# Optimization experiments

Measured on AMD Instinct MI355X. Metric: run time of the kernel, lower is better.

## Reference

```python
import jax, jax.numpy as jnp
import numpy as np

DIM = 512; HEADS = 8; DH = 64; M = 256; ITERS = 6; N_PATCH = 10000; N_CLASSES = 2


def layernorm(x, w, b, eps=1e-5):
    mu = x.mean(-1, keepdims=True)
    var = ((x - mu) ** 2).mean(-1, keepdims=True)
    return (x - mu) * jax.lax.rsqrt(var + eps) * w + b


def pinv_iter(x, iters=ITERS):
    # Moore-Penrose iterative pseudo-inverse (lucidrains nystrom-attention)
    abs_x = jnp.abs(x)
    col = abs_x.sum(-1)
    row = abs_x.sum(-2)
    z = jnp.swapaxes(x, -1, -2) / (jnp.max(col) * jnp.max(row))
    I = jnp.eye(x.shape[-1], dtype=x.dtype)
    for _ in range(iters):
        xz = x @ z
        z = 0.25 * z @ (13 * I - xz @ (15 * I - xz @ (7 * I - xz)))
    return z


def nystrom_attn(x, qkv_w, out_w, out_b, res_w):
    b, n, _ = x.shape
    pad = (-n) % M  # front-pad so n divisible by num_landmarks
    xp = jnp.pad(x, ((0, 0), (pad, 0), (0, 0)))
    npad = n + pad
    qkv = (xp @ qkv_w).reshape(b, npad, 3, HEADS, DH)
    q = jnp.transpose(qkv[:, :, 0], (0, 2, 1, 3)) * (DH ** -0.5)  # [b,h,n,d]
    k = jnp.transpose(qkv[:, :, 1], (0, 2, 1, 3))
    v = jnp.transpose(qkv[:, :, 2], (0, 2, 1, 3))
    l = npad // M
    q_l = q.reshape(b, HEADS, M, l, DH).mean(3)  # landmark means [b,h,m,d]
    k_l = k.reshape(b, HEADS, M, l, DH).mean(3)
    attn1 = jax.nn.softmax(jnp.einsum('bhnd,bhmd->bhnm', q, k_l), -1)
    attn2 = jax.nn.softmax(jnp.einsum('bhid,bhjd->bhij', q_l, k_l), -1)
    attn3 = jax.nn.softmax(jnp.einsum('bhmd,bhnd->bhmn', q_l, k), -1)
    out = (attn1 @ pinv_iter(attn2)) @ (attn3 @ v)  # [b,h,n,d]
    pk = (res_w.shape[2] - 1) // 2
    out = out + jax.lax.conv_general_dilated(
        v, res_w, (1, 1), [(pk, pk), (0, 0)], feature_group_count=HEADS)
    out = jnp.transpose(out, (0, 2, 1, 3)).reshape(b, npad, HEADS * DH)
    out = out @ out_w + out_b
    return out[:, -n:]


def ppeg(x, H, W, w7, b7, w5, b5, w3, b3):
    B, _, C = x.shape
    cls_tok, feat = x[:, :1], x[:, 1:]
    f = jnp.transpose(feat, (0, 2, 1)).reshape(B, C, H, W)
    def dw(w, b):
        p = w.shape[2] // 2
        return jax.lax.conv_general_dilated(
            f, w, (1, 1), [(p, p), (p, p)], feature_group_count=C) + b[None, :, None, None]
    y = f + dw(w7, b7) + dw(w5, b5) + dw(w3, b3)
    y = jnp.transpose(y.reshape(B, C, H * W), (0, 2, 1))
    return jnp.concatenate([cls_tok, y], axis=1)


def setup_inputs() -> dict:
    key = jax.random.key(0)
    ks = jax.random.split(key, 16)
    d = {
        'x': jax.random.normal(ks[0], (1, N_PATCH, DIM), jnp.float32),
        'cls_token': jax.random.normal(ks[1], (1, 1, DIM), jnp.float32) * 1e-6,
        'ln1_w': jnp.ones((DIM,), jnp.float32), 'ln1_b': jnp.zeros((DIM,), jnp.float32),
        'qkv1_w': jax.random.normal(ks[2], (DIM, 3 * DIM), jnp.float32) * 0.03,
        'out1_w': jax.random.normal(ks[3], (DIM, DIM), jnp.float32) * 0.04,
        'out1_b': jnp.zeros((DIM,), jnp.float32),
        'res1_w': jax.random.normal(ks[4], (HEADS, 1, 33, 1), jnp.float32) * 0.1,
        'p7_w': jax.random.normal(ks[5], (DIM, 1, 7, 7), jnp.float32) * 0.1,
        'p7_b': jnp.zeros((DIM,), jnp.float32),
        'p5_w': jax.random.normal(ks[6], (DIM, 1, 5, 5), jnp.float32) * 0.1,
        'p5_b': jnp.zeros((DIM,), jnp.float32),
        'p3_w': jax.random.normal(ks[7], (DIM, 1, 3, 3), jnp.float32) * 0.1,
        'p3_b': jnp.zeros((DIM,), jnp.float32),
        'ln2_w': jnp.ones((DIM,), jnp.float32), 'ln2_b': jnp.zeros((DIM,), jnp.float32),
        'qkv2_w': jax.random.normal(ks[8], (DIM, 3 * DIM), jnp.float32) * 0.03,
        'out2_w': jax.random.normal(ks[9], (DIM, DIM), jnp.float32) * 0.04,
        'out2_b': jnp.zeros((DIM,), jnp.float32),
        'res2_w': jax.random.normal(ks[10], (HEADS, 1, 33, 1), jnp.float32) * 0.1,
        'norm_w': jnp.ones((DIM,), jnp.float32), 'norm_b': jnp.zeros((DIM,), jnp.float32),
        'fc2_w': jax.random.normal(ks[11], (DIM, N_CLASSES), jnp.float32) * 0.06,
        'fc2_b': jnp.zeros((N_CLASSES,), jnp.float32),
        'pc_w': jax.random.normal(ks[12], (DIM, N_CLASSES), jnp.float32) * 0.06,
        'pc_b': jnp.zeros((N_CLASSES,), jnp.float32),
    }
    return d


def reference(x, cls_token, ln1_w, ln1_b, qkv1_w, out1_w, out1_b, res1_w,
              p7_w, p7_b, p5_w, p5_b, p3_w, p3_b,
              ln2_w, ln2_b, qkv2_w, out2_w, out2_b, res2_w,
              norm_w, norm_b, fc2_w, fc2_b, pc_w, pc_b):
    h = x.astype(jnp.float32)
    B, n0, C = h.shape
    _H = int(np.ceil(np.sqrt(n0))); _W = _H
    add = _H * _W - n0
    if add > 0:
        h = jnp.concatenate([h, h[:, :add]], axis=1)
    h = jnp.concatenate([jnp.broadcast_to(cls_token, (B, 1, C)), h], axis=1)
    h = h + nystrom_attn(layernorm(h, ln1_w, ln1_b), qkv1_w, out1_w, out1_b, res1_w)
    h = ppeg(h, _H, _W, p7_w, p7_b, p5_w, p5_b, p3_w, p3_b)
    h = h + nystrom_attn(layernorm(h, ln2_w, ln2_b), qkv2_w, out2_w, out2_b, res2_w)
    hn = layernorm(h, norm_w, norm_b)
    cls_f = hn[:, 0]
    patch_f = hn[:, 1:]
    if add > 0:
        patch_f = patch_f[:, :n0]
    bag_logits = cls_f @ fc2_w + fc2_b
    patch_logits = patch_f @ pc_w + pc_b
    patch_scores = jax.nn.softmax(patch_logits, -1)
    return bag_logits, patch_logits, patch_scores
```

## Files before the change

kernel.cpp:

```cpp
#include <hip/hip_runtime.h>
#include <hip/hip_bf16.h>

#define DIM    512
#define HEADS  8
#define DHD    64
#define MLAND  256
#define NTOK   10001
#define NPATCH 10000
#define NPAD   10240
#define PADR   239
#define LFAC   40
#define MOUT   10112
#define NSPLIT 8

typedef __bf16 bf16x8_t __attribute__((ext_vector_type(8)));
typedef float  f32x4_t  __attribute__((ext_vector_type(4)));
typedef short  short8_t __attribute__((ext_vector_type(8)));

__device__ inline bf16x8_t bzero8() {
    union { short8_t s; bf16x8_t b; } u;
    u.s = (short8_t){0, 0, 0, 0, 0, 0, 0, 0};
    return u.b;
}

#define GLDS(gp, lp) __builtin_amdgcn_global_load_lds( \
    (const __attribute__((address_space(1))) void*)(gp), \
    (__attribute__((address_space(3))) void*)(lp), 16, 0, 0)

__global__ void k_concat(const float* __restrict__ x, const float* __restrict__ cls,
                         float* __restrict__ h) {
    int idx = blockIdx.x * 256 + threadIdx.x;
    if (idx >= NTOK * DIM) return;
    int row = idx / DIM, col = idx % DIM;
    h[idx] = (row == 0) ? cls[col] : x[(row - 1) * DIM + col];
}

__global__ void k_layernorm_bf(const float* __restrict__ h, const float* __restrict__ w,
                               const float* __restrict__ b, __hip_bfloat16* __restrict__ xbf) {
    int row = blockIdx.x;
    const float* r = h + (long)row * DIM;
    int t = threadIdx.x;
    float v0 = r[t], v1 = r[t + 256];
    __shared__ float red[256];
    red[t] = v0 + v1; __syncthreads();
    for (int o = 128; o > 0; o >>= 1) { if (t < o) red[t] += red[t + o]; __syncthreads(); }
    float mu = red[0] * (1.f / DIM); __syncthreads();
    float d0 = v0 - mu, d1 = v1 - mu;
    red[t] = d0 * d0 + d1 * d1; __syncthreads();
    for (int o = 128; o > 0; o >>= 1) { if (t < o) red[t] += red[t + o]; __syncthreads(); }
    float rstd = rsqrtf(red[0] * (1.f / DIM) + 1e-5f);
    long base = (long)(PADR + row) * DIM;
    xbf[base + t]       = __float2bfloat16(d0 * rstd * w[t] + b[t]);
    xbf[base + t + 256] = __float2bfloat16(d1 * rstd * w[t + 256] + b[t + 256]);
}

__global__ void k_zerobf(__hip_bfloat16* __restrict__ p, int n) {
    int i = blockIdx.x * 256 + threadIdx.x;
    if (i < n) p[i] = __float2bfloat16(0.f);
}
__global__ void k_wt_cvt(const float* __restrict__ W, __hip_bfloat16* __restrict__ Wt,
                         int K, int N) {
    __shared__ float tile[32][33];
    int k0 = blockIdx.x * 32, n0 = blockIdx.y * 32;
    int lx = threadIdx.x % 32, ly = threadIdx.x / 32;
    for (int i = 0; i < 32; i += 8) tile[ly + i][lx] = W[(long)(k0 + ly + i) * N + n0 + lx];
    __syncthreads();
    for (int i = 0; i < 32; i += 8)
        Wt[(long)(n0 + ly + i) * K + k0 + lx] = __float2bfloat16(tile[lx][ly + i]);
}
__global__ void k_vt(const __hip_bfloat16* __restrict__ vh, __hip_bfloat16* __restrict__ vt) {
    __shared__ __hip_bfloat16 tile[32][33];
    int n0 = blockIdx.x * 32, d0 = blockIdx.y * 32, h = blockIdx.z;
    int lx = threadIdx.x % 32, ly = threadIdx.x / 32;
    for (int i = 0; i < 32; i += 8)
        tile[ly + i][lx] = vh[((long)h * NPAD + n0 + ly + i) * 64 + d0 + lx];
    __syncthreads();
    for (int i = 0; i < 32; i += 8)
        vt[((long)h * 64 + d0 + ly + i) * NPAD + n0 + lx] = tile[lx][ly + i];
}

__global__ __launch_bounds__(256) void k_qkv_gemm(
    const __hip_bfloat16* __restrict__ A, const __hip_bfloat16* __restrict__ Bt,
    __hip_bfloat16* __restrict__ qh, __hip_bfloat16* __restrict__ kh,
    __hip_bfloat16* __restrict__ vh)
{
    const int K = 512;
    __shared__ unsigned short As[2][128 * 64];
    __shared__ unsigned short Bs[2][128 * 64];
    int tid = threadIdx.x;
    int m0 = blockIdx.y * 128, n0 = blockIdx.x * 128;
    int wave = tid >> 6, lane = tid & 63;
    int wm = (wave & 1) * 64, wn = (wave >> 1) * 64;
    f32x4_t zero4 = {0.f, 0.f, 0.f, 0.f};
    f32x4_t acc[4][4];
#pragma unroll
    for (int i = 0; i < 4; i++)
#pragma unroll
        for (int j = 0; j < 4; j++) acc[i][j] = zero4;
    int quad = lane >> 4, fr = lane & 15;
    int lrow8 = lane >> 3, gls = lane & 7;
    int gg = gls ^ lrow8;

#define STAGE_AB(K0, AD, BD) do { \
    _Pragma("unroll") \
    for (int rnd = 0; rnd < 4; rnd++) { \
        int r0 = rnd * 32 + wave * 8; \
        int ar = r0 + lrow8; \
        GLDS(A  + (long)(m0 + ar) * K + (K0) + gg * 8, (AD) + r0 * 64); \
        GLDS(Bt + (long)(n0 + ar) * K + (K0) + gg * 8, (BD) + r0 * 64); \
    } \
} while (0)

    STAGE_AB(0, &As[0][0], &Bs[0][0]);
    for (int k0 = 0; k0 < K; k0 += 64) {
        int b = (k0 >> 6) & 1;
        if (k0 + 64 < K) {
            STAGE_AB(k0 + 64, &As[b ^ 1][0], &Bs[b ^ 1][0]);
            asm volatile("s_waitcnt vmcnt(8)" ::: "memory");
        } else {
            asm volatile("s_waitcnt vmcnt(0)" ::: "memory");
        }
        __builtin_amdgcn_s_barrier();
#pragma unroll
        for (int ks = 0; ks < 2; ks++) {
            int sg = (ks * 4 + quad) ^ (fr & 7);
            bf16x8_t af[4], bq[4];
#pragma unroll
            for (int i = 0; i < 4; i++) {
                af[i] = *(const bf16x8_t*)&As[b][(wm + i * 16 + fr) * 64 + sg * 8];
                bq[i] = *(const bf16x8_t*)&Bs[b][(wn + i * 16 + fr) * 64 + sg * 8];
            }
#pragma unroll
            for (int i = 0; i < 4; i++)
#pragma unroll
                for (int j = 0; j < 4; j++)
                    acc[i][j] = __builtin_amdgcn_mfma_f32_16x16x32_bf16(af[i], bq[j], acc[i][j], 0, 0, 0);
        }
        asm volatile("" ::: "memory");
        __builtin_amdgcn_s_barrier();
    }
#undef STAGE_AB
    int col = lane & 15, rq = lane >> 4;
#pragma unroll
    for (int j = 0; j < 4; j++) {
        int c = n0 + wn + j * 16 + col;
        int sect = c >> 9;
        int hh = (c >> 6) & 7;
        int d = c & 63;
        __hip_bfloat16* dst = (sect == 0) ? qh : (sect == 1) ? kh : vh;
        float sc = (sect == 0) ? 0.125f : 1.f;
#pragma unroll
        for (int i = 0; i < 4; i++) {
            int rbase = m0 + wm + i * 16 + rq * 4;
#pragma unroll
            for (int rr = 0; rr < 4; rr++) {
                int r = rbase + rr;
                dst[((long)hh * NPAD + r) * 64 + d] = __float2bfloat16(acc[i][j][rr] * sc);
            }
        }
    }
}

__global__ __launch_bounds__(256) void k_mfma_gemm(
    const __hip_bfloat16* __restrict__ A, const __hip_bfloat16* __restrict__ Bt,
    float* __restrict__ C, int M, int N, int K, int Mstore,
    const float* __restrict__ bias, int accum)
{
    __shared__ unsigned short As[2][128 * 64];
    __shared__ unsigned short Bs[2][128 * 64];
    int tid = threadIdx.x;
    int m0 = blockIdx.y * 128, n0 = blockIdx.x * 128;
    int wave = tid >> 6, lane = tid & 63;
    int wm = (wave & 1) * 64, wn = (wave >> 1) * 64;
    f32x4_t zero4 = {0.f, 0.f, 0.f, 0.f};
    f32x4_t acc[4][4];
#pragma unroll
    for (int i = 0; i < 4; i++)
#pragma unroll
        for (int j = 0; j < 4; j++) acc[i][j] = zero4;
    int quad = lane >> 4, fr = lane & 15;
    int lrow8 = lane >> 3, gls = lane & 7;
    int gg = gls ^ lrow8;

#define STAGE_AB(K0, AD, BD) do { \
    _Pragma("unroll") \
    for (int rnd = 0; rnd < 4; rnd++) { \
        int r0 = rnd * 32 + wave * 8; \
        int ar = r0 + lrow8; \
        GLDS(A  + (long)(m0 + ar) * K + (K0) + gg * 8, (AD) + r0 * 64); \
        GLDS(Bt + (long)(n0 + ar) * K + (K0) + gg * 8, (BD) + r0 * 64); \
    } \
} while (0)

    STAGE_AB(0, &As[0][0], &Bs[0][0]);
    for (int k0 = 0; k0 < K; k0 += 64) {
        int b = (k0 >> 6) & 1;
        if (k0 + 64 < K) {
            STAGE_AB(k0 + 64, &As[b ^ 1][0], &Bs[b ^ 1][0]);
            asm volatile("s_waitcnt vmcnt(8)" ::: "memory");
        } else {
            asm volatile("s_waitcnt vmcnt(0)" ::: "memory");
        }
        __builtin_amdgcn_s_barrier();
#pragma unroll
        for (int ks = 0; ks < 2; ks++) {
            int sg = (ks * 4 + quad) ^ (fr & 7);
            bf16x8_t af[4], bq[4];
#pragma unroll
            for (int i = 0; i < 4; i++) {
                af[i] = *(const bf16x8_t*)&As[b][(wm + i * 16 + fr) * 64 + sg * 8];
                bq[i] = *(const bf16x8_t*)&Bs[b][(wn + i * 16 + fr) * 64 + sg * 8];
            }
#pragma unroll
            for (int i = 0; i < 4; i++)
#pragma unroll
                for (int j = 0; j < 4; j++)
                    acc[i][j] = __builtin_amdgcn_mfma_f32_16x16x32_bf16(af[i], bq[j], acc[i][j], 0, 0, 0);
        }
        asm volatile("" ::: "memory");
        __builtin_amdgcn_s_barrier();
    }
#undef STAGE_AB
    int col = lane & 15, rq = lane >> 4;
#pragma unroll
    for (int j = 0; j < 4; j++) {
        int c = n0 + wn + j * 16 + col;
        float bsv = bias ? bias[c] : 0.f;
#pragma unroll
        for (int i = 0; i < 4; i++) {
            int rbase = m0 + wm + i * 16 + rq * 4;
#pragma unroll
            for (int rr = 0; rr < 4; rr++) {
                int r = rbase + rr;
                if (r >= Mstore) continue;
                float v = acc[i][j][rr] + bsv;
                long off = (long)r * N + c;
                if (accum) C[off] += v; else C[off] = v;
            }
        }
    }
}

__global__ __launch_bounds__(256) void k_mfma_t64(
    const __hip_bfloat16* __restrict__ A, long lda, long abatch, int arowmax,
    const __hip_bfloat16* __restrict__ Bt, long ldb, long bbatch,
    __hip_bfloat16* __restrict__ Cbf, long ldc, long cbatch, int ksplit)
{
    int h = blockIdx.z;
    const __hip_bfloat16* Ab = A + (long)h * abatch;
    const __hip_bfloat16* Bb = Bt + (long)h * bbatch;
    int m0 = blockIdx.y * 128;
    int kbeg = blockIdx.x * ksplit, kend = kbeg + ksplit;
    int wave = threadIdx.x >> 6, lane = threadIdx.x & 63;
    int wm = (wave & 1) * 64, wn = (wave >> 1) * 32;
    int fr = lane & 15, quad = lane >> 4;
    f32x4_t zero4 = {0.f, 0.f, 0.f, 0.f};
    f32x4_t acc[4][2];
#pragma unroll
    for (int i = 0; i < 4; i++) { acc[i][0] = zero4; acc[i][1] = zero4; }
    for (int k0 = kbeg; k0 < kend; k0 += 32) {
        bf16x8_t bq[2];
#pragma unroll
        for (int j = 0; j < 2; j++)
            bq[j] = *(const bf16x8_t*)(Bb + (long)(wn + j * 16 + fr) * ldb + k0 + quad * 8);
#pragma unroll
        for (int i = 0; i < 4; i++) {
            int r = m0 + wm + i * 16 + fr;
            bf16x8_t af = (r < arowmax) ? *(const bf16x8_t*)(Ab + (long)r * lda + k0 + quad * 8)
                                        : bzero8();
#pragma unroll
            for (int j = 0; j < 2; j++)
                acc[i][j] = __builtin_amdgcn_mfma_f32_16x16x32_bf16(af, bq[j], acc[i][j], 0, 0, 0);
        }
    }
#pragma unroll
    for (int i = 0; i < 4; i++)
#pragma unroll
        for (int j = 0; j < 2; j++)
#pragma unroll
            for (int rr = 0; rr < 4; rr++) {
                int r = m0 + wm + i * 16 + quad * 4 + rr;
                int c = wn + j * 16 + fr;
                Cbf[(long)h * cbatch + (long)c * ldc + r] = __float2bfloat16(acc[i][j][rr]);
            }
}

__global__ __launch_bounds__(256) void k_mm256(
    const __hip_bfloat16* __restrict__ Aa, const __hip_bfloat16* __restrict__ Bt,
    float s, float acoef, const __hip_bfloat16* __restrict__ Aadd,
    __hip_bfloat16* __restrict__ Ca, __hip_bfloat16* __restrict__ Ct)
{
    int hd = blockIdx.z;
    long hb = (long)hd * 65536;
    int m0 = blockIdx.y * 64, n0 = blockIdx.x * 32;
    int wave = threadIdx.x >> 6, lane = threadIdx.x & 63;
    int fr = lane & 15, quad = lane >> 4;
    int mrow = m0 + wave * 16;
    f32x4_t zero4 = {0.f, 0.f, 0.f, 0.f};
    f32x4_t acc[2];
    acc[0] = zero4; acc[1] = zero4;
#pragma unroll
    for (int k0 = 0; k0 < 256; k0 += 32) {
        bf16x8_t af = *(const bf16x8_t*)(Aa + hb + (long)(mrow + fr) * 256 + k0 + quad * 8);
#pragma unroll
        for (int j = 0; j < 2; j++) {
            bf16x8_t bq = *(const bf16x8_t*)(Bt + hb + (long)(n0 + j * 16 + fr) * 256 + k0 + quad * 8);
            acc[j] = __builtin_amdgcn_mfma_f32_16x16x32_bf16(af, bq, acc[j], 0, 0, 0);
        }
    }
#pragma unroll
    for (int j = 0; j < 2; j++)
#pragma unroll
        for (int rr = 0; rr < 4; rr++) {
            int r = mrow + quad * 4 + rr;
            int c = n0 + j * 16 + fr;
            float v = s * acc[j][rr];
            if (Aadd) v += acoef * __bfloat162float(Aadd[hb + (long)r * 256 + c]);
            __hip_bfloat16 bv = __float2bfloat16(v);
            if (Ca) Ca[hb + (long)r * 256 + c] = bv;
            if (Ct) Ct[hb + (long)c * 256 + r] = bv;
        }
}

__global__ __launch_bounds__(256) void k_attn3f(
    const __hip_bfloat16* __restrict__ qlbf, const __hip_bfloat16* __restrict__ kh,
    const __hip_bfloat16* __restrict__ vt, float* __restrict__ part)
{
    int ns = blockIdx.x, mt = blockIdx.y, h = blockIdx.z;
    int wave = threadIdx.x >> 6, lane = threadIdx.x & 63;
    int fr = lane & 15, quad = lane >> 4;
    int lrow8 = lane >> 3, gls = lane & 7;
    int gg = gls ^ lrow8;
    int vsub = lane >> 5, vgrp = lane & 31;
    int swz = fr & 7;
    __shared__ unsigned short Ks[2][256 * 64];
    __shared__ unsigned short Vs[2][64 * 256];
    __shared__ __hip_bfloat16 Pl[64 * 136];
    f32x4_t zero4 = {0.f, 0.f, 0.f, 0.f};
    bf16x8_t aq[2];
    {
        const __hip_bfloat16* qb = qlbf + (long)h * 16384 + (long)(mt * 64 + wave * 16 + fr) * 64;
        aq[0] = *(const bf16x8_t*)(qb + quad * 8);
        aq[1] = *(const bf16x8_t*)(qb + 32 + quad * 8);
    }
    f32x4_t O[4];
#pragma unroll
    for (int j = 0; j < 4; j++) O[j] = zero4;
    float mr[4] = {-1e30f, -1e30f, -1e30f, -1e30f};
    float lr[4] = {0.f, 0.f, 0.f, 0.f};
    const __hip_bfloat16* kb = kh + (long)h * NPAD * 64;
    const __hip_bfloat16* vb = vt + (long)h * 64 * NPAD;

#define STAGE_KV(N0, KD, VD) do { \
    _Pragma("unroll") \
    for (int rnd = 0; rnd < 8; rnd++) { \
        int r0 = rnd * 32 + wave * 8; \
        GLDS(kb + (long)((N0) + r0 + lrow8) * 64 + gg * 8, (KD) + r0 * 64); \
    } \
    _Pragma("unroll") \
    for (int rnd = 0; rnd < 8; rnd++) { \
        int v0 = rnd * 8 + wave * 2; \
        int vrow = v0 + vsub; \
        GLDS(vb + (long)vrow * NPAD + (N0) + (vgrp ^ (vrow & 7)) * 8, (VD) + v0 * 256); \
    } \
} while (0)

    STAGE_KV(ns * 1280, &Ks[0][0], &Vs[0][0]);

    for (int nt = 0; nt < 5; nt++) {
        int bsel = nt & 1;
        if (nt < 4) {
            int n1 = ns * 1280 + (nt + 1) * 256;
            STAGE_KV(n1, &Ks[bsel ^ 1][0], &Vs[bsel ^ 1][0]);
            asm volatile("s_waitcnt vmcnt(16)" ::: "memory");
        } else {
            asm volatile("s_waitcnt vmcnt(0)" ::: "memory");
        }
        __builtin_amdgcn_s_barrier();

        const unsigned short* Kc = &Ks[bsel][0];
        const unsigned short* Vc = &Vs[bsel][0];
        f32x4_t s[16];
#pragma unroll
        for (int j = 0; j < 16; j++) s[j] = zero4;
#pragma unroll
        for (int j = 0; j < 16; j++) {
            const unsigned short* kr = Kc + (j * 16 + fr) * 64;
            bf16x8_t b0 = *(const bf16x8_t*)(kr + (quad ^ swz) * 8);
            bf16x8_t b1 = *(const bf16x8_t*)(kr + ((quad ^ swz) ^ 4) * 8);
            s[j] = __builtin_amdgcn_mfma_f32_16x16x32_bf16(aq[0], b0, s[j], 0, 0, 0);
            s[j] = __builtin_amdgcn_mfma_f32_16x16x32_bf16(aq[1], b1, s[j], 0, 0, 0);
        }
        float tm[4] = {-1e30f, -1e30f, -1e30f, -1e30f};
#pragma unroll
        for (int j = 0; j < 16; j++)
#pragma unroll
            for (int rr = 0; rr < 4; rr++) tm[rr] = fmaxf(tm[rr], s[j][rr]);
#pragma unroll
        for (int rr = 0; rr < 4; rr++) {
#pragma unroll
            for (int o = 8; o > 0; o >>= 1) tm[rr] = fmaxf(tm[rr], __shfl_xor(tm[rr], o));
        }
        float alpha[4], ts[4];
#pragma unroll
        for (int rr = 0; rr < 4; rr++) {
            float mnew = fmaxf(mr[rr], tm[rr]);
            alpha[rr] = __expf(mr[rr] - mnew);
            mr[rr] = mnew;
            ts[rr] = 0.f;
        }
#pragma unroll
        for (int j = 0; j < 16; j++)
#pragma unroll
            for (int rr = 0; rr < 4; rr++) {
                float e = __expf(s[j][rr] - mr[rr]);
                s[j][rr] = e;
                ts[rr] += e;
            }
#pragma unroll
        for (int rr = 0; rr < 4; rr++) {
#pragma unroll
            for (int o = 8; o > 0; o >>= 1) ts[rr] += __shfl_xor(ts[rr], o);
            lr[rr] = lr[rr] * alpha[rr] + ts[rr];
        }
#pragma unroll
        for (int j = 0; j < 4; j++)
#pragma unroll
            for (int rr = 0; rr < 4; rr++) O[j][rr] *= alpha[rr];
#pragma unroll
        for (int half = 0; half < 2; half++) {
#pragma unroll
            for (int j = 0; j < 8; j++)
#pragma unroll
                for (int rr = 0; rr < 4; rr++)
                    Pl[(wave * 16 + quad * 4 + rr) * 136 + j * 16 + fr] =
                        __float2bfloat16(s[half * 8 + j][rr]);
#pragma unroll
            for (int k0 = 0; k0 < 128; k0 += 32) {
                bf16x8_t af = *(const bf16x8_t*)&Pl[(wave * 16 + fr) * 136 + k0 + quad * 8];
                int gb = (half * 128 + k0) >> 3;
#pragma unroll
                for (int j = 0; j < 4; j++) {
                    const unsigned short* vr = Vc + (j * 16 + fr) * 256;
                    bf16x8_t bq = *(const bf16x8_t*)(vr + ((gb + quad) ^ swz) * 8);
                    O[j] = __builtin_amdgcn_mfma_f32_16x16x32_bf16(af, bq, O[j], 0, 0, 0);
                }
            }
        }
        asm volatile("" ::: "memory");
        __builtin_amdgcn_s_barrier();
    }
#undef STAGE_KV

    float* Ob = part + (long)((h * 4 + mt) * NSPLIT + ns) * 4224;
#pragma unroll
    for (int j = 0; j < 4; j++)
#pragma unroll
        for (int rr = 0; rr < 4; rr++)
            Ob[(wave * 16 + quad * 4 + rr) * 64 + j * 16 + fr] = O[j][rr];
    if (fr == 0) {
#pragma unroll
        for (int rr = 0; rr < 4; rr++) {
            Ob[4096 + wave * 16 + quad * 4 + rr] = mr[rr];
            Ob[4160 + wave * 16 + quad * 4 + rr] = lr[rr];
        }
    }
}

__global__ void k_a3comb(const float* __restrict__ part, __hip_bfloat16* __restrict__ a3vt) {
    int mt = blockIdx.x, h = blockIdx.y, t = threadIdx.x;
    int row = t >> 2, c0 = (t & 3) * 16;
    long base = (long)((h * 4 + mt) * NSPLIT) * 4224;
    float M = -1e30f;
    for (int s = 0; s < NSPLIT; s++) M = fmaxf(M, part[base + s * 4224 + 4096 + row]);
    float L = 0.f;
    float o[16];
#pragma unroll
    for (int c = 0; c < 16; c++) o[c] = 0.f;
    for (int s = 0; s < NSPLIT; s++) {
        const float* pb = part + base + (long)s * 4224;
        float w = __expf(pb[4096 + row] - M);
        L += pb[4160 + row] * w;
#pragma unroll
        for (int c = 0; c < 16; c++) o[c] += w * pb[row * 64 + c0 + c];
    }
    float invL = 1.f / L;
#pragma unroll
    for (int c = 0; c < 16; c++)
        a3vt[(long)h * 16384 + (long)(c0 + c) * 256 + mt * 64 + row] = __float2bfloat16(o[c] * invL);
}

__global__ void k_conv_res(const __hip_bfloat16* __restrict__ vh, const float* __restrict__ resw,
                           __hip_bfloat16* __restrict__ convbf) {
    int e4 = blockIdx.x * 256 + threadIdx.x;
    if (e4 >= NTOK * 128) return;
    int i = e4 >> 7;
    int c4 = (e4 & 127) * 4;
    int hh = c4 >> 6, d = c4 & 63;
    int n = PADR + i;
    const __hip_bfloat16* vb = vh + (long)hh * NPAD * 64 + d;
    float a0 = 0.f, a1 = 0.f, a2 = 0.f, a3 = 0.f;
#pragma unroll
    for (int t = 0; t < 33; t++) {
        int nn = n - 16 + t;
        if (nn < NPAD) {
            float w = resw[hh * 33 + t];
            uint2 pv = *(const uint2*)(vb + (long)nn * 64);
            __hip_bfloat16 vv[4];
            *(uint2*)vv = pv;
            a0 += w * __bfloat162float(vv[0]);
            a1 += w * __bfloat162float(vv[1]);
            a2 += w * __bfloat162float(vv[2]);
            a3 += w * __bfloat162float(vv[3]);
        }
    }
    __hip_bfloat16 o[4] = {__float2bfloat16(a0), __float2bfloat16(a1),
                           __float2bfloat16(a2), __float2bfloat16(a3)};
    *(uint2*)(convbf + (long)i * DIM + c4) = *(uint2*)o;
}

__global__ __launch_bounds__(256, 3) void k_attn1f(
    const __hip_bfloat16* __restrict__ qh, const __hip_bfloat16* __restrict__ klbf,
    const __hip_bfloat16* __restrict__ w2bt, const __hip_bfloat16* __restrict__ convbf,
    __hip_bfloat16* __restrict__ abf)
{
    int h = blockIdx.y;
    int i0 = blockIdx.x * 64;
    __shared__ __hip_bfloat16 Pl[64 * 136];
    __shared__ float mS[2][2][2][16];
    int tid = threadIdx.x;
    int wave = tid >> 6, lane = tid & 63;
    int rg = wave & 1, lh = wave >> 1;
    int fr = lane & 15, quad = lane >> 4;
    const __hip_bfloat16* kb = klbf + (long)h * (MLAND * DHD) + (long)lh * 128 * DHD;
    f32x4_t zero4 = {0.f, 0.f, 0.f, 0.f};

    f32x4_t s0[8], s1[8];
#pragma unroll
    for (int j = 0; j < 8; j++) { s0[j] = zero4; s1[j] = zero4; }
    int arow0 = i0 + rg * 16 + fr;
    int arow1 = arow0 + 32;
    const __hip_bfloat16* qrow = qh + ((long)h * NPAD + PADR + arow0) * 64;
#pragma unroll
    for (int k0 = 0; k0 < 64; k0 += 32) {
        bf16x8_t af0 = (arow0 < NTOK) ? *(const bf16x8_t*)(qrow + k0 + quad * 8) : bzero8();
        bf16x8_t af1 = (arow1 < NTOK) ? *(const bf16x8_t*)(qrow + 32 * 64 + k0 + quad * 8) : bzero8();
#pragma unroll
        for (int j = 0; j < 8; j++) {
            bf16x8_t bq = *(const bf16x8_t*)(kb + (long)(j * 16 + fr) * DHD + k0 + quad * 8);
            s0[j] = __builtin_amdgcn_mfma_f32_16x16x32_bf16(af0, bq, s0[j], 0, 0, 0);
            s1[j] = __builtin_amdgcn_mfma_f32_16x16x32_bf16(af1, bq, s1[j], 0, 0, 0);
        }
    }
    float sum0[4] = {0.f, 0.f, 0.f, 0.f}, sum1[4] = {0.f, 0.f, 0.f, 0.f};
#pragma unroll
    for (int j = 0; j < 8; j++)
#pragma unroll
        for (int rr = 0; rr < 4; rr++) {
            float e0 = __expf(s0[j][rr]); s0[j][rr] = e0; sum0[rr] += e0;
            float e1 = __expf(s1[j][rr]); s1[j][rr] = e1; sum1[rr] += e1;
        }
#pragma unroll
    for (int rr = 0; rr < 4; rr++) {
#pragma unroll
        for (int o = 8; o > 0; o >>= 1) {
            sum0[rr] += __shfl_xor(sum0[rr], o);
            sum1[rr] += __shfl_xor(sum1[rr], o);
        }
    }
    if (fr == 0) {
#pragma unroll
        for (int rr = 0; rr < 4; rr++) {
            mS[0][lh][rg][quad * 4 + rr] = sum0[rr];
            mS[1][lh][rg][quad * 4 + rr] = sum1[rr];
        }
    }
#pragma unroll
    for (int j = 0; j < 8; j++)
#pragma unroll
        for (int rr = 0; rr < 4; rr++) {
            Pl[(rg * 16 + quad * 4 + rr) * 136 + j * 16 + fr]      = __float2bfloat16(s0[j][rr]);
            Pl[(32 + rg * 16 + quad * 4 + rr) * 136 + j * 16 + fr] = __float2bfloat16(s1[j][rr]);
        }
    __syncthreads();
    float fac0[4], fac1[4];
#pragma unroll
    for (int rr = 0; rr < 4; rr++) {
        fac0[rr] = 1.f / (sum0[rr] + mS[0][lh ^ 1][rg][quad * 4 + rr]);
        fac1[rr] = 1.f / (sum1[rr] + mS[1][lh ^ 1][rg][quad * 4 + rr]);
    }
    float cp[2][4][4];
    if (lh == 0) {
#pragma unroll
        for (int rt = 0; rt < 2; rt++)
#pragma unroll
            for (int j = 0; j < 4; j++)
#pragma unroll
                for (int rr = 0; rr < 4; rr++) {
                    int r = i0 + rt * 32 + rg * 16 + quad * 4 + rr;
                    cp[rt][j][rr] = (r < NTOK)
                        ? __bfloat162float(convbf[(long)r * DIM + h * DHD + j * 16 + fr]) : 0.f;
                }
    }
    const __hip_bfloat16* wb = w2bt + (long)h * (DHD * MLAND) + lh * 128;
    f32x4_t oc0[4], oc1[4];
#pragma unroll
    for (int j = 0; j < 4; j++) { oc0[j] = zero4; oc1[j] = zero4; }
#pragma unroll
    for (int k0 = 0; k0 < 128; k0 += 32) {
        bf16x8_t af0 = *(const bf16x8_t*)&Pl[(rg * 16 + fr) * 136 + k0 + quad * 8];
        bf16x8_t af1 = *(const bf16x8_t*)&Pl[(32 + rg * 16 + fr) * 136 + k0 + quad * 8];
#pragma unroll
        for (int j = 0; j < 4; j++) {
            bf16x8_t bq = *(const bf16x8_t*)(wb + (long)(j * 16 + fr) * MLAND + k0 + quad * 8);
            oc0[j] = __builtin_amdgcn_mfma_f32_16x16x32_bf16(af0, bq, oc0[j], 0, 0, 0);
            oc1[j] = __builtin_amdgcn_mfma_f32_16x16x32_bf16(af1, bq, oc1[j], 0, 0, 0);
        }
    }
#pragma unroll
    for (int j = 0; j < 4; j++)
#pragma unroll
        for (int rr = 0; rr < 4; rr++) {
            oc0[j][rr] *= fac0[rr];
            oc1[j][rr] *= fac1[rr];
        }
    __syncthreads();
    float* ex = (float*)Pl;
    if (lh == 1) {
#pragma unroll
        for (int j = 0; j < 4; j++)
#pragma unroll
            for (int rr = 0; rr < 4; rr++) {
                ex[(rg * 16 + quad * 4 + rr) * 64 + j * 16 + fr]      = oc0[j][rr];
                ex[(32 + rg * 16 + quad * 4 + rr) * 64 + j * 16 + fr] = oc1[j][rr];
            }
    }
    __syncthreads();
    if (lh == 0) {
#pragma unroll
        for (int j = 0; j < 4; j++)
#pragma unroll
            for (int rr = 0; rr < 4; rr++) {
                int lr0 = rg * 16 + quad * 4 + rr;
                int r0 = i0 + lr0;
                if (r0 < NTOK) {
                    float v = oc0[j][rr] + ex[lr0 * 64 + j * 16 + fr] + cp[0][j][rr];
                    abf[(long)r0 * DIM + h * DHD + j * 16 + fr] = __float2bfloat16(v);
                }
                int r1 = r0 + 32;
                if (r1 < NTOK) {
                    float v = oc1[j][rr] + ex[(32 + lr0) * 64 + j * 16 + fr] + cp[1][j][rr];
                    abf[(long)r1 * DIM + h * DHD + j * 16 + fr] = __float2bfloat16(v);
                }
            }
    }
}

__global__ void k_landmarks(const __hip_bfloat16* __restrict__ qh,
                            const __hip_bfloat16* __restrict__ kh,
                            float* __restrict__ ql, float* __restrict__ kl,
                            __hip_bfloat16* __restrict__ qlbf, __hip_bfloat16* __restrict__ klbf) {
    int m = blockIdx.x, h = blockIdx.y, d = threadIdx.x;
    float sq = 0.f, sk = 0.f;
    for (int j = 0; j < LFAC; j++) {
        long base = ((long)h * NPAD + m * LFAC + j) * 64 + d;
        sq += __bfloat162float(qh[base]);
        sk += __bfloat162float(kh[base]);
    }
    long o = ((long)h * MLAND + m) * DHD + d;
    float vq = sq * (1.f / LFAC), vk = sk * (1.f / LFAC);
    ql[o] = vq; kl[o] = vk;
    qlbf[o] = __float2bfloat16(vq);
    klbf[o] = __float2bfloat16(vk);
}

__global__ void k_attn2(const float* __restrict__ ql, const float* __restrict__ kl,
                        float* __restrict__ attn2, __hip_bfloat16* __restrict__ attn2bf) {
    int i = blockIdx.x, h = blockIdx.y, j = threadIdx.x;
    __shared__ float q[64];
    __shared__ float red[256];
    if (j < 64) q[j] = ql[((long)h * MLAND + i) * DHD + j];
    __syncthreads();
    const float* kr = kl + ((long)h * MLAND + j) * DHD;
    float s = 0.f;
#pragma unroll 8
    for (int d = 0; d < 64; d++) s += q[d] * kr[d];
    red[j] = s; __syncthreads();
    for (int o = 128; o > 0; o >>= 1) { if (j < o) red[j] = fmaxf(red[j], red[j + o]); __syncthreads(); }
    float mx = red[0]; __syncthreads();
    float e = __expf(s - mx);
    red[j] = e; __syncthreads();
    for (int o = 128; o > 0; o >>= 1) { if (j < o) red[j] += red[j + o]; __syncthreads(); }
    float v = e / red[0];
    long off = ((long)h * MLAND + i) * MLAND + j;
    attn2[off] = v;
    attn2bf[off] = __float2bfloat16(v);
}

__global__ void k_colrow(const float* __restrict__ x, float* __restrict__ scal) {
    int h = blockIdx.x, t = threadIdx.x;
    const float* xh = x + (long)h * MLAND * MLAND;
    float cs = 0.f, rs = 0.f;
    for (int j = 0; j < MLAND; j++) {
        cs += fabsf(xh[(long)t * MLAND + j]);
        rs += fabsf(xh[(long)j * MLAND + t]);
    }
    __shared__ float red[256];
    red[t] = cs; __syncthreads();
    for (int o = 128; o > 0; o >>= 1) { if (t < o) red[t] = fmaxf(red[t], red[t + o]); __syncthreads(); }
    if (t == 0) scal[2 + h] = red[0];
    __syncthreads();
    red[t] = rs; __syncthreads();
    for (int o = 128; o > 0; o >>= 1) { if (t < o) red[t] = fmaxf(red[t], red[t + o]); __syncthreads(); }
    if (t == 0) scal[10 + h] = red[0];
}

__global__ void k_tscale2(const float* __restrict__ x, const float* __restrict__ scal,
                          __hip_bfloat16* __restrict__ za, __hip_bfloat16* __restrict__ zt) {
    int h = blockIdx.z;
    int tj = blockIdx.x * 32, ti = blockIdx.y * 32;
    __shared__ float tile[32][33];
    const float* xh = x + (long)h * 65536;
    int lx = threadIdx.x % 32, ly = threadIdx.x / 32;
    float cm = scal[2], rm = scal[10];
#pragma unroll
    for (int k = 1; k < 8; k++) {
        cm = fmaxf(cm, scal[2 + k]);
        rm = fmaxf(rm, scal[10 + k]);
    }
    float inv = 1.f / (cm * rm);
    for (int yy = 0; yy < 32; yy += 8) {
        float v = xh[(long)(ti + ly + yy) * MLAND + tj + lx];
        tile[ly + yy][lx] = v;
        zt[(long)h * 65536 + (long)(ti + ly + yy) * MLAND + tj + lx] = __float2bfloat16(v * inv);
    }
    __syncthreads();
    for (int yy = 0; yy < 32; yy += 8)
        za[(long)h * 65536 + (long)(tj + ly + yy) * MLAND + ti + lx] =
            __float2bfloat16(tile[lx][ly + yy] * inv);
}

__global__ void k_tfwd(const float* __restrict__ h, float* __restrict__ ft) {
    __shared__ float tile[32][33];
    int t0 = blockIdx.x * 32, c0 = blockIdx.y * 32;
    int lx = threadIdx.x % 32, ly = threadIdx.x / 32;
    for (int i = 0; i < 32; i += 8) {
        int t = t0 + ly + i;
        if (t < NPATCH) tile[ly + i][lx] = h[(long)(1 + t) * DIM + c0 + lx];
    }
    __syncthreads();
    for (int i = 0; i < 32; i += 8) {
        int c = c0 + ly + i, t = t0 + lx;
        if (t < NPATCH) ft[(long)c * NPATCH + t] = tile[lx][ly + i];
    }
}

__global__ __launch_bounds__(256) void k_ppeg2(
    const float* __restrict__ ft, float* __restrict__ yt,
    const float* __restrict__ w7, const float* __restrict__ b7,
    const float* __restrict__ w5, const float* __restrict__ b5,
    const float* __restrict__ w3, const float* __restrict__ b3)
{
    int s = blockIdx.x, c = blockIdx.y;
    __shared__ float tile[26][106];
    __shared__ float wt[49];
    int tid = threadIdx.x;
    int r0 = s * 20 - 3;
    for (int idx = tid; idx < 26 * 106; idx += 256) {
        int rr = idx / 106, cc = idx % 106;
        int gy = r0 + rr, gx = cc - 3;
        float v = 0.f;
        if (gy >= 0 && gy < 100 && gx >= 0 && gx < 100)
            v = ft[(long)c * NPATCH + gy * 100 + gx];
        tile[rr][cc] = v;
    }
    if (tid < 49) {
        int dy = tid / 7 - 3, dx = tid % 7 - 3;
        float w = w7[c * 49 + tid];
        if (dy >= -2 && dy <= 2 && dx >= -2 && dx <= 2) w += w5[c * 25 + (dy + 2) * 5 + (dx + 2)];
        if (dy >= -1 && dy <= 1 && dx >= -1 && dx <= 1) w += w3[c * 9 + (dy + 1) * 3 + (dx + 1)];
        wt[tid] = w;
    }
    __syncthreads();
    float bsum = b7[c] + b5[c] + b3[c];
    for (int p = tid; p < 2000; p += 256) {
        int ly = p / 100, lx = p % 100;
        float acc = tile[ly + 3][lx + 3] + bsum;
#pragma unroll
        for (int dy = 0; dy < 7; dy++)
#pragma unroll
            for (int dx = 0; dx < 7; dx++)
                acc += wt[dy * 7 + dx] * tile[ly + dy][lx + dx];
        yt[(long)c * NPATCH + (s * 20 + ly) * 100 + lx] = acc;
    }
}

__global__ void k_tback(const float* __restrict__ yt, float* __restrict__ h) {
    __shared__ float tile[32][33];
    int t0 = blockIdx.x * 32, c0 = blockIdx.y * 32;
    int lx = threadIdx.x % 32, ly = threadIdx.x / 32;
    for (int i = 0; i < 32; i += 8) {
        int c = c0 + ly + i, t = t0 + lx;
        if (t < NPATCH) tile[ly + i][lx] = yt[(long)c * NPATCH + t];
    }
    __syncthreads();
    for (int i = 0; i < 32; i += 8) {
        int t = t0 + ly + i;
        if (t < NPATCH) h[(long)(1 + t) * DIM + c0 + lx] = tile[lx][ly + i];
    }
}

__global__ void k_final(const float* __restrict__ h, const float* __restrict__ nw,
                        const float* __restrict__ nb,
                        const float* __restrict__ fc2w, const float* __restrict__ fc2b,
                        const float* __restrict__ pcw, const float* __restrict__ pcb,
                        float* __restrict__ out)
{
    int row = blockIdx.x;
    int t = threadIdx.x;
    const float* r = h + (long)row * DIM;
    float v0 = r[t], v1 = r[t + 256];
    __shared__ float red[256];
    red[t] = v0 + v1; __syncthreads();
    for (int o = 128; o > 0; o >>= 1) { if (t < o) red[t] += red[t + o]; __syncthreads(); }
    float mu = red[0] * (1.f / DIM); __syncthreads();
    float d0 = v0 - mu, d1 = v1 - mu;
    red[t] = d0 * d0 + d1 * d1; __syncthreads();
    for (int o = 128; o > 0; o >>= 1) { if (t < o) red[t] += red[t + o]; __syncthreads(); }
    float rstd = rsqrtf(red[0] * (1.f / DIM) + 1e-5f); __syncthreads();
    float h0 = d0 * rstd * nw[t] + nb[t];
    float h1 = d1 * rstd * nw[t + 256] + nb[t + 256];
    const float* w = (row == 0) ? fc2w : pcw;
    float p0 = h0 * w[t * 2] + h1 * w[(t + 256) * 2];
    float p1 = h0 * w[t * 2 + 1] + h1 * w[(t + 256) * 2 + 1];
    red[t] = p0; __syncthreads();
    for (int o = 128; o > 0; o >>= 1) { if (t < o) red[t] += red[t + o]; __syncthreads(); }
    float l0 = red[0]; __syncthreads();
    red[t] = p1; __syncthreads();
    for (int o = 128; o > 0; o >>= 1) { if (t < o) red[t] += red[t + o]; __syncthreads(); }
    if (t == 0) {
        float l1 = red[0];
        const float* bb = (row == 0) ? fc2b : pcb;
        float a0 = l0 + bb[0], a1 = l1 + bb[1];
        if (row == 0) { out[0] = a0; out[1] = a1; }
        else {
            long i = row - 1;
            out[2 + i * 2] = a0;
            out[2 + i * 2 + 1] = a1;
            float m = fmaxf(a0, a1);
            float e0 = __expf(a0 - m), e1 = __expf(a1 - m);
            float inv = 1.f / (e0 + e1);
            out[2 + 2 * NPATCH + i * 2] = e0 * inv;
            out[2 + 2 * NPATCH + i * 2 + 1] = e1 * inv;
        }
    }
}

extern "C" void kernel_launch(void* const* d_in, const int* in_sizes, int n_in,
                              void* d_out, int out_size, void* d_ws, size_t ws_size,
                              hipStream_t stream)
{
    const float* x     = (const float*)d_in[0];
    const float* cls   = (const float*)d_in[1];
    const float* ln1w  = (const float*)d_in[2];
    const float* ln1b  = (const float*)d_in[3];
    const float* qkv1w = (const float*)d_in[4];
    const float* out1w = (const float*)d_in[5];
    const float* out1b = (const float*)d_in[6];
    const float* res1w = (const float*)d_in[7];
    const float* p7w   = (const float*)d_in[8];
    const float* p7b   = (const float*)d_in[9];
    const float* p5w   = (const float*)d_in[10];
    const float* p5b   = (const float*)d_in[11];
    const float* p3w   = (const float*)d_in[12];
    const float* p3b   = (const float*)d_in[13];
    const float* ln2w  = (const float*)d_in[14];
    const float* ln2b  = (const float*)d_in[15];
    const float* qkv2w = (const float*)d_in[16];
    const float* out2w = (const float*)d_in[17];
    const float* out2b = (const float*)d_in[18];
    const float* res2w = (const float*)d_in[19];
    const float* normw = (const float*)d_in[20];
    const float* normb = (const float*)d_in[21];
    const float* fc2w  = (const float*)d_in[22];
    const float* fc2b  = (const float*)d_in[23];
    const float* pcw   = (const float*)d_in[24];
    const float* pcb   = (const float*)d_in[25];
    float* out = (float*)d_out;

    float* p = (float*)d_ws;
    float* h      = p; p += 5120512;
    float* yt     = p; p += 5120512;
    float* ql     = p; p += 131072;
    float* kl     = p; p += 131072;
    float* x2     = p; p += 524288;
    float* scal   = p; p += 32;
    float* part   = p; p += 1081344;
    float* ft     = p; p += 5120512;
    __hip_bfloat16* qh     = (__hip_bfloat16*)p; p += 2621440;
    __hip_bfloat16* kh     = (__hip_bfloat16*)p; p += 2621440;
    __hip_bfloat16* vh     = (__hip_bfloat16*)p; p += 2621440;
    __hip_bfloat16* xbf    = (__hip_bfloat16*)p; p += 2621440;
    __hip_bfloat16* abf    = (__hip_bfloat16*)p; p += 2588672;
    __hip_bfloat16* convbf = (__hip_bfloat16*)p; p += 2560256;
    __hip_bfloat16* qw1t   = (__hip_bfloat16*)p; p += 393216;
    __hip_bfloat16* qw2t   = (__hip_bfloat16*)p; p += 393216;
    __hip_bfloat16* ow1t   = (__hip_bfloat16*)p; p += 131072;
    __hip_bfloat16* ow2t   = (__hip_bfloat16*)p; p += 131072;
    __hip_bfloat16* x2a    = (__hip_bfloat16*)p; p += 262144;
    __hip_bfloat16* za     = (__hip_bfloat16*)p; p += 262144;
    __hip_bfloat16* zt     = (__hip_bfloat16*)p; p += 262144;
    __hip_bfloat16* za2    = (__hip_bfloat16*)p; p += 262144;
    __hip_bfloat16* zt2    = (__hip_bfloat16*)p; p += 262144;
    __hip_bfloat16* xza    = (__hip_bfloat16*)p; p += 262144;
    __hip_bfloat16* xzt    = (__hip_bfloat16*)p; p += 262144;
    __hip_bfloat16* t1t    = (__hip_bfloat16*)p; p += 262144;
    __hip_bfloat16* t2t    = (__hip_bfloat16*)p; p += 262144;
    __hip_bfloat16* qlbf   = (__hip_bfloat16*)p; p += 65536;
    __hip_bfloat16* klbf   = (__hip_bfloat16*)p; p += 65536;
    __hip_bfloat16* vt     = (__hip_bfloat16*)p; p += 2621440;
    __hip_bfloat16* a3vt   = (__hip_bfloat16*)p; p += 65536;
    __hip_bfloat16* w2bt   = (__hip_bfloat16*)p; p += 65536;

    k_concat<<<dim3((NTOK * DIM + 255) / 256), 256, 0, stream>>>(x, cls, h);
    k_wt_cvt<<<dim3(16, 48), 256, 0, stream>>>(qkv1w, qw1t, 512, 1536);
    k_wt_cvt<<<dim3(16, 48), 256, 0, stream>>>(qkv2w, qw2t, 512, 1536);
    k_wt_cvt<<<dim3(16, 16), 256, 0, stream>>>(out1w, ow1t, 512, 512);
    k_wt_cvt<<<dim3(16, 16), 256, 0, stream>>>(out2w, ow2t, 512, 512);
    k_zerobf<<<dim3((PADR * DIM + 255) / 256), 256, 0, stream>>>(xbf, PADR * DIM);

    auto layer = [&](const float* lnw, const float* lnb, const __hip_bfloat16* qwt,
                     const __hip_bfloat16* owt, const float* outb, const float* resw) {
        k_layernorm_bf<<<NTOK, 256, 0, stream>>>(h, lnw, lnb, xbf);
        k_qkv_gemm<<<dim3(12, 80), 256, 0, stream>>>(xbf, qwt, qh, kh, vh);
        k_vt<<<dim3(320, 2, HEADS), 256, 0, stream>>>(vh, vt);
        k_landmarks<<<dim3(MLAND, HEADS), 64, 0, stream>>>(qh, kh, ql, kl, qlbf, klbf);
        k_attn2<<<dim3(MLAND, HEADS), 256, 0, stream>>>(ql, kl, x2, x2a);
        k_colrow<<<HEADS, 256, 0, stream>>>(x2, scal);
        k_tscale2<<<dim3(8, 8, HEADS), 256, 0, stream>>>(x2, scal, za, zt);
        {
            __hip_bfloat16 *zra = za, *zrt = zt, *zoa = za2, *zot = zt2;
            dim3 g(8, 4, HEADS);
            for (int it = 0; it < 6; it++) {
                k_mm256<<<g, 256, 0, stream>>>(x2a, zrt, 1.f, 0.f, nullptr, xza, xzt);
                k_mm256<<<g, 256, 0, stream>>>(xza, xzt, -1.f, 7.f, xza, nullptr, t1t);
                k_mm256<<<g, 256, 0, stream>>>(xza, t1t, -1.f, 15.f, xza, nullptr, t2t);
                k_mm256<<<g, 256, 0, stream>>>(zra, t2t, -0.25f, 3.25f, zra, zoa, zot);
                __hip_bfloat16* tmp;
                tmp = zra; zra = zoa; zoa = tmp;
                tmp = zrt; zrt = zot; zot = tmp;
            }
        }
        k_attn3f<<<dim3(NSPLIT, 4, HEADS), 256, 0, stream>>>(qlbf, kh, vt, part);
        k_a3comb<<<dim3(4, HEADS), 256, 0, stream>>>(part, a3vt);
        k_mfma_t64<<<dim3(1, 2, HEADS), 256, 0, stream>>>(
            za, 256, 65536, 256, a3vt, 256, 16384,
            w2bt, 256, 16384, 256);
        k_conv_res<<<dim3((NTOK * 128 + 255) / 256), 256, 0, stream>>>(vh, resw, convbf);
        k_attn1f<<<dim3(157, HEADS), 256, 0, stream>>>(qh, klbf, w2bt, convbf, abf);
        k_mfma_gemm<<<dim3(4, 79), 256, 0, stream>>>(abf, owt, h, MOUT, 512, 512,
                                                     NTOK, outb, 1);
    };

    layer(ln1w, ln1b, qw1t, ow1t, out1b, res1w);

    k_tfwd<<<dim3(313, 16), 256, 0, stream>>>(h, ft);
    k_ppeg2<<<dim3(5, 512), 256, 0, stream>>>(ft, yt, p7w, p7b, p5w, p5b, p3w, p3b);
    k_tback<<<dim3(313, 16), 256, 0, stream>>>(yt, h);

    layer(ln2w, ln2b, qw2t, ow2t, out2b, res2w);

    k_final<<<NTOK, 256, 0, stream>>>(h, normw, normb, fc2w, fc2b, pcw, pcb, out);
    (void)in_sizes; (void)n_in; (void)out_size; (void)ws_size;
}
```

Baseline: 965.8 us.

## Restructure pinv iteration into parallel products and use wave-per-row layernorm

Rewrites each Newton-Schulz pseudo-inverse step as z·xz and xz·xz computed in one launch, then a fused kernel forming 3.25z-3.75U+1.75U·xz-0.25U·W. This cuts the serial matmul chain per iteration from four launches to three. Layernorm and the final head kernel now process one row per wavefront with shuffle reductions instead of block-wide shared-memory trees. The column-abs-sum max is replaced by 1.0, relying on softmax rows summing to one, which changes bf16 rounding slightly.

```diff
diff --git a/kernel.cpp b/kernel.cpp
--- a/kernel.cpp
+++ b/kernel.cpp
@@ -35,23 +35,34 @@
     h[idx] = (row == 0) ? cls[col] : x[(row - 1) * DIM + col];
 }
 
-__global__ void k_layernorm_bf(const float* __restrict__ h, const float* __restrict__ w,
-                               const float* __restrict__ b, __hip_bfloat16* __restrict__ xbf) {
-    int row = blockIdx.x;
+__global__ __launch_bounds__(256) void k_layernorm_bf(
+    const float* __restrict__ h, const float* __restrict__ w,
+    const float* __restrict__ b, __hip_bfloat16* __restrict__ xbf) {
+    int wave = threadIdx.x >> 6, lane = threadIdx.x & 63;
+    int row = blockIdx.x * 4 + wave;
+    if (row >= NTOK) return;
     const float* r = h + (long)row * DIM;
-    int t = threadIdx.x;
-    float v0 = r[t], v1 = r[t + 256];
-    __shared__ float red[256];
-    red[t] = v0 + v1; __syncthreads();
-    for (int o = 128; o > 0; o >>= 1) { if (t < o) red[t] += red[t + o]; __syncthreads(); }
-    float mu = red[0] * (1.f / DIM); __syncthreads();
-    float d0 = v0 - mu, d1 = v1 - mu;
-    red[t] = d0 * d0 + d1 * d1; __syncthreads();
-    for (int o = 128; o > 0; o >>= 1) { if (t < o) red[t] += red[t + o]; __syncthreads(); }
-    float rstd = rsqrtf(red[0] * (1.f / DIM) + 1e-5f);
-    long base = (long)(PADR + row) * DIM;
-    xbf[base + t]       = __float2bfloat16(d0 * rstd * w[t] + b[t]);
-    xbf[base + t + 256] = __float2bfloat16(d1 * rstd * w[t + 256] + b[t + 256]);
+    int c0 = lane * 8;
+    f32x4_t va = *(const f32x4_t*)(r + c0);
+    f32x4_t vb = *(const f32x4_t*)(r + c0 + 4);
+    float s = va[0] + va[1] + va[2] + va[3] + vb[0] + vb[1] + vb[2] + vb[3];
+#pragma unroll
+    for (int o = 32; o > 0; o >>= 1) s += __shfl_xor(s, o);
+    float mu = s * (1.f / DIM);
+    float d[8];
+#pragma unroll
+    for (int i = 0; i < 4; i++) { d[i] = va[i] - mu; d[4 + i] = vb[i] - mu; }
+    float vs = 0.f;
+#pragma unroll
+    for (int i = 0; i < 8; i++) vs += d[i] * d[i];
+#pragma unroll
+    for (int o = 32; o > 0; o >>= 1) vs += __shfl_xor(vs, o);
+    float rstd = rsqrtf(vs * (1.f / DIM) + 1e-5f);
+    __hip_bfloat16 ob[8];
+#pragma unroll
+    for (int i = 0; i < 8; i++)
+        ob[i] = __float2bfloat16(d[i] * rstd * w[c0 + i] + b[c0 + i]);
+    *(uint4*)(xbf + (long)(PADR + row) * DIM + c0) = *(uint4*)ob;
 }
 
 __global__ void k_zerobf(__hip_bfloat16* __restrict__ p, int n) {
@@ -319,6 +330,83 @@
             __hip_bfloat16 bv = __float2bfloat16(v);
             if (Ca) Ca[hb + (long)r * 256 + c] = bv;
             if (Ct) Ct[hb + (long)c * 256 + r] = bv;
+        }
+}
+
+__global__ __launch_bounds__(256) void k_pinvUW(
+    const __hip_bfloat16* __restrict__ za, const __hip_bfloat16* __restrict__ xza,
+    const __hip_bfloat16* __restrict__ xzt,
+    __hip_bfloat16* __restrict__ ua, __hip_bfloat16* __restrict__ wt)
+{
+    int z = blockIdx.z;
+    int hd = z & 7, isW = z >> 3;
+    long hb = (long)hd * 65536;
+    int m0 = blockIdx.y * 64, n0 = blockIdx.x * 32;
+    int wave = threadIdx.x >> 6, lane = threadIdx.x & 63;
+    int fr = lane & 15, quad = lane >> 4;
+    int mrow = m0 + wave * 16;
+    const __hip_bfloat16* Aa = isW ? xza : za;
+    f32x4_t zero4 = {0.f, 0.f, 0.f, 0.f};
+    f32x4_t acc[2];
+    acc[0] = zero4; acc[1] = zero4;
+#pragma unroll
+    for (int k0 = 0; k0 < 256; k0 += 32) {
+        bf16x8_t af = *(const bf16x8_t*)(Aa + hb + (long)(mrow + fr) * 256 + k0 + quad * 8);
+#pragma unroll
+        for (int j = 0; j < 2; j++) {
+            bf16x8_t bq = *(const bf16x8_t*)(xzt + hb + (long)(n0 + j * 16 + fr) * 256 + k0 + quad * 8);
+            acc[j] = __builtin_amdgcn_mfma_f32_16x16x32_bf16(af, bq, acc[j], 0, 0, 0);
+        }
+    }
+#pragma unroll
+    for (int j = 0; j < 2; j++)
+#pragma unroll
+        for (int rr = 0; rr < 4; rr++) {
+            int r = mrow + quad * 4 + rr;
+            int c = n0 + j * 16 + fr;
+            __hip_bfloat16 bv = __float2bfloat16(acc[j][rr]);
+            if (!isW) ua[hb + (long)r * 256 + c] = bv;
+            else      wt[hb + (long)c * 256 + r] = bv;
+        }
+}
+
+__global__ __launch_bounds__(256) void k_pinv3(
+    const __hip_bfloat16* __restrict__ ua, const __hip_bfloat16* __restrict__ xzt,
+    const __hip_bfloat16* __restrict__ wt, const __hip_bfloat16* __restrict__ za,
+    __hip_bfloat16* __restrict__ Ca, __hip_bfloat16* __restrict__ Ct)
+{
+    int hd = blockIdx.z;
+    long hb = (long)hd * 65536;
+    int m0 = blockIdx.y * 64, n0 = blockIdx.x * 32;
+    int wave = threadIdx.x >> 6, lane = threadIdx.x & 63;
+    int fr = lane & 15, quad = lane >> 4;
+    int mrow = m0 + wave * 16;
+    f32x4_t zero4 = {0.f, 0.f, 0.f, 0.f};
+    f32x4_t acc1[2], acc2[2];
+    acc1[0] = zero4; acc1[1] = zero4; acc2[0] = zero4; acc2[1] = zero4;
+#pragma unroll
+    for (int k0 = 0; k0 < 256; k0 += 32) {
+        bf16x8_t af = *(const bf16x8_t*)(ua + hb + (long)(mrow + fr) * 256 + k0 + quad * 8);
+#pragma unroll
+        for (int j = 0; j < 2; j++) {
+            bf16x8_t b1 = *(const bf16x8_t*)(xzt + hb + (long)(n0 + j * 16 + fr) * 256 + k0 + quad * 8);
+            bf16x8_t b2 = *(const bf16x8_t*)(wt  + hb + (long)(n0 + j * 16 + fr) * 256 + k0 + quad * 8);
+            acc1[j] = __builtin_amdgcn_mfma_f32_16x16x32_bf16(af, b1, acc1[j], 0, 0, 0);
+            acc2[j] = __builtin_amdgcn_mfma_f32_16x16x32_bf16(af, b2, acc2[j], 0, 0, 0);
+        }
+    }
+#pragma unroll
+    for (int j = 0; j < 2; j++)
+#pragma unroll
+        for (int rr = 0; rr < 4; rr++) {
+            int r = mrow + quad * 4 + rr;
+            int c = n0 + j * 16 + fr;
+            float zv = __bfloat162float(za[hb + (long)r * 256 + c]);
+            float uv = __bfloat162float(ua[hb + (long)r * 256 + c]);
+            float v = 3.25f * zv - 3.75f * uv + 1.75f * acc1[j][rr] - 0.25f * acc2[j][rr];
+            __hip_bfloat16 bv = __float2bfloat16(v);
+            Ca[hb + (long)r * 256 + c] = bv;
+            Ct[hb + (long)c * 256 + r] = bv;
         }
 }
 
@@ -700,19 +788,12 @@
 __global__ void k_colrow(const float* __restrict__ x, float* __restrict__ scal) {
     int h = blockIdx.x, t = threadIdx.x;
     const float* xh = x + (long)h * MLAND * MLAND;
-    float cs = 0.f, rs = 0.f;
-    for (int j = 0; j < MLAND; j++) {
-        cs += fabsf(xh[(long)t * MLAND + j]);
-        rs += fabsf(xh[(long)j * MLAND + t]);
-    }
+    float rs = 0.f;
+    for (int j = 0; j < MLAND; j++) rs += fabsf(xh[(long)j * MLAND + t]);
     __shared__ float red[256];
-    red[t] = cs; __syncthreads();
-    for (int o = 128; o > 0; o >>= 1) { if (t < o) red[t] = fmaxf(red[t], red[t + o]); __syncthreads(); }
-    if (t == 0) scal[2 + h] = red[0];
-    __syncthreads();
     red[t] = rs; __syncthreads();
     for (int o = 128; o > 0; o >>= 1) { if (t < o) red[t] = fmaxf(red[t], red[t + o]); __syncthreads(); }
-    if (t == 0) scal[10 + h] = red[0];
+    if (t == 0) { scal[10 + h] = red[0]; scal[2 + h] = 1.0f; }
 }
 
 __global__ void k_tscale2(const float* __restrict__ x, const float* __restrict__ scal,
@@ -810,38 +891,49 @@
     }
 }
 
-__global__ void k_final(const float* __restrict__ h, const float* __restrict__ nw,
-                        const float* __restrict__ nb,
-                        const float* __restrict__ fc2w, const float* __restrict__ fc2b,
-                        const float* __restrict__ pcw, const float* __restrict__ pcb,
-                        float* __restrict__ out)
+__global__ __launch_bounds__(256) void k_final(
+    const float* __restrict__ h, const float* __restrict__ nw,
+    const float* __restrict__ nb,
+    const float* __restrict__ fc2w, const float* __restrict__ fc2b,
+    const float* __restrict__ pcw, const float* __restrict__ pcb,
+    float* __restrict__ out)
 {
-    int row = blockIdx.x;
-    int t = threadIdx.x;
+    int wave = threadIdx.x >> 6, lane = threadIdx.x & 63;
+    int row = blockIdx.x * 4 + wave;
+    if (row >= NTOK) return;
     const float* r = h + (long)row * DIM;
-    float v0 = r[t], v1 = r[t + 256];
-    __shared__ float red[256];
-    red[t] = v0 + v1; __syncthreads();
-    for (int o = 128; o > 0; o >>= 1) { if (t < o) red[t] += red[t + o]; __syncthreads(); }
-    float mu = red[0] * (1.f / DIM); __syncthreads();
-    float d0 = v0 - mu, d1 = v1 - mu;
-    red[t] = d0 * d0 + d1 * d1; __syncthreads();
-    for (int o = 128; o > 0; o >>= 1) { if (t < o) red[t] += red[t + o]; __syncthreads(); }
-    float rstd = rsqrtf(red[0] * (1.f / DIM) + 1e-5f); __syncthreads();
-    float h0 = d0 * rstd * nw[t] + nb[t];
-    float h1 = d1 * rstd * nw[t + 256] + nb[t + 256];
+    int c0 = lane * 8;
+    f32x4_t va = *(const f32x4_t*)(r + c0);
+    f32x4_t vb = *(const f32x4_t*)(r + c0 + 4);
+    float s = va[0] + va[1] + va[2] + va[3] + vb[0] + vb[1] + vb[2] + vb[3];
+#pragma unroll
+    for (int o = 32; o > 0; o >>= 1) s += __shfl_xor(s, o);
+    float mu = s * (1.f / DIM);
+    float d[8];
+#pragma unroll
+    for (int i = 0; i < 4; i++) { d[i] = va[i] - mu; d[4 + i] = vb[i] - mu; }
+    float vs = 0.f;
+#pragma unroll
+    for (int i = 0; i < 8; i++) vs += d[i] * d[i];
+#pragma unroll
+    for (int o = 32; o > 0; o >>= 1) vs += __shfl_xor(vs, o);
+    float rstd = rsqrtf(vs * (1.f / DIM) + 1e-5f);
     const float* w = (row == 0) ? fc2w : pcw;
-    float p0 = h0 * w[t * 2] + h1 * w[(t + 256) * 2];
-    float p1 = h0 * w[t * 2 + 1] + h1 * w[(t + 256) * 2 + 1];
-    red[t] = p0; __syncthreads();
-    for (int o = 128; o > 0; o >>= 1) { if (t < o) red[t] += red[t + o]; __syncthreads(); }
-    float l0 = red[0]; __syncthreads();
-    red[t] = p1; __syncthreads();
-    for (int o = 128; o > 0; o >>= 1) { if (t < o) red[t] += red[t + o]; __syncthreads(); }
-    if (t == 0) {
-        float l1 = red[0];
+    float p0 = 0.f, p1 = 0.f;
+#pragma unroll
+    for (int i = 0; i < 8; i++) {
+        float hn = d[i] * rstd * nw[c0 + i] + nb[c0 + i];
+        p0 += hn * w[(c0 + i) * 2];
+        p1 += hn * w[(c0 + i) * 2 + 1];
+    }
+#pragma unroll
+    for (int o = 32; o > 0; o >>= 1) {
+        p0 += __shfl_xor(p0, o);
+        p1 += __shfl_xor(p1, o);
+    }
+    if (lane == 0) {
         const float* bb = (row == 0) ? fc2b : pcb;
-        float a0 = l0 + bb[0], a1 = l1 + bb[1];
+        float a0 = p0 + bb[0], a1 = p1 + bb[1];
         if (row == 0) { out[0] = a0; out[1] = a1; }
         else {
             long i = row - 1;
@@ -931,7 +1023,7 @@
 
     auto layer = [&](const float* lnw, const float* lnb, const __hip_bfloat16* qwt,
                      const __hip_bfloat16* owt, const float* outb, const float* resw) {
-        k_layernorm_bf<<<NTOK, 256, 0, stream>>>(h, lnw, lnb, xbf);
+        k_layernorm_bf<<<dim3((NTOK + 3) / 4), 256, 0, stream>>>(h, lnw, lnb, xbf);
         k_qkv_gemm<<<dim3(12, 80), 256, 0, stream>>>(xbf, qwt, qh, kh, vh);
         k_vt<<<dim3(320, 2, HEADS), 256, 0, stream>>>(vh, vt);
         k_landmarks<<<dim3(MLAND, HEADS), 64, 0, stream>>>(qh, kh, ql, kl, qlbf, klbf);
@@ -940,12 +1032,11 @@
         k_tscale2<<<dim3(8, 8, HEADS), 256, 0, stream>>>(x2, scal, za, zt);
         {
             __hip_bfloat16 *zra = za, *zrt = zt, *zoa = za2, *zot = zt2;
-            dim3 g(8, 4, HEADS);
+            dim3 g(8, 4, HEADS), g2(8, 4, 16);
             for (int it = 0; it < 6; it++) {
                 k_mm256<<<g, 256, 0, stream>>>(x2a, zrt, 1.f, 0.f, nullptr, xza, xzt);
-                k_mm256<<<g, 256, 0, stream>>>(xza, xzt, -1.f, 7.f, xza, nullptr, t1t);
-                k_mm256<<<g, 256, 0, stream>>>(xza, t1t, -1.f, 15.f, xza, nullptr, t2t);
-                k_mm256<<<g, 256, 0, stream>>>(zra, t2t, -0.25f, 3.25f, zra, zoa, zot);
+                k_pinvUW<<<g2, 256, 0, stream>>>(zra, xza, xzt, t1t, t2t);
+                k_pinv3<<<g, 256, 0, stream>>>(t1t, xzt, t2t, zra, zoa, zot);
                 __hip_bfloat16* tmp;
                 tmp = zra; zra = zoa; zoa = tmp;
                 tmp = zrt; zrt = zot; zot = tmp;
@@ -970,6 +1061,6 @@
 
     layer(ln2w, ln2b, qw2t, ow2t, out2b, res2w);
 
-    k_final<<<NTOK, 256, 0, stream>>>(h, normw, normb, fc2w, fc2b, pcw, pcb, out);
+    k_final<<<dim3((NTOK + 3) / 4), 256, 0, stream>>>(h, normw, normb, fc2w, fc2b, pcw, pcb, out);
     (void)in_sizes; (void)n_in; (void)out_size; (void)ws_size;
 }
```

Result: faster. 877.8 us (-9.1%).
